# Optimization experiments

Hardware: AMD Instinct MI355X
Metric: run time of the kernel (lower is better)

Reference implementation:

```python
import jax, jax.numpy as jnp
import numpy as np

N, E, DIN, H, M, O = 100000, 3200000, 128, 256, 500, 100


def setup_inputs() -> dict:
    key = jax.random.key(0)
    ks = jax.random.split(key, 8)
    x = jax.random.normal(ks[0], (N, DIN), dtype=jnp.float32)
    edge_index = jax.random.randint(ks[1], (2, E), 0, N, dtype=jnp.int64)
    # GCNConv weights (glorot-ish scale) and biases
    W1 = jax.random.normal(ks[2], (DIN, H), dtype=jnp.float32) / np.sqrt(DIN)
    b1 = jnp.zeros((H,), dtype=jnp.float32)
    W2 = jax.random.normal(ks[3], (H, M), dtype=jnp.float32) / np.sqrt(H)
    b2 = jnp.zeros((M,), dtype=jnp.float32)
    # output head ('GO'): Linear(M -> O)
    Wout = jax.random.normal(ks[4], (M, O), dtype=jnp.float32) / np.sqrt(M)
    bout = jnp.zeros((O,), dtype=jnp.float32)
    # threshold param stored as inv_softplus(1.0) so softplus(threshold)=1.0
    threshold = jnp.float32(np.log(np.expm1(1.0)))
    return {"x": x, "edge_index": edge_index, "W1": W1, "b1": b1,
            "W2": W2, "b2": b2, "Wout": Wout, "bout": bout,
            "threshold": threshold}


def reference(x, edge_index, W1, b1, W2, b2, Wout, bout, threshold):
    src, dst = edge_index[0], edge_index[1]
    n = x.shape[0]
    # GCN sym-normalization with improved=True (self-loop weight 2):
    # deg[i] = 2 + #incoming edges; norm(e) = deg^-1/2[src] * deg^-1/2[dst]
    deg = jax.ops.segment_sum(jnp.ones(src.shape[0], x.dtype), dst,
                              num_segments=n) + jnp.asarray(2.0, x.dtype)
    dinv = jax.lax.rsqrt(deg)
    coef = dinv[src] * dinv[dst]              # [E]
    self_coef = (2.0 * dinv * dinv)[:, None]  # [N,1] self-loop term

    def gcn_conv(h, W, b):
        h = h @ W                              # [N,C]
        agg = jax.ops.segment_sum(h[src] * coef[:, None], dst, num_segments=n)
        return agg + self_coef * h + b

    h = jax.nn.relu(gcn_conv(x, W1, b1))       # conv + ReLU (no bn, no dropout)
    module_representation = jax.nn.softplus(gcn_conv(h, W2, b2))  # [N,M]
    # tanh probability transform: tanh(softplus(threshold) * x)
    p = jnp.tanh(jax.nn.softplus(threshold) * module_representation)
    y_go = p @ Wout + bout                     # output head 'GO'
    return (module_representation, y_go)
```

## Files before the change

kernel.cpp:

```cpp
#include <hip/hip_runtime.h>
#include <cstdint>
#include <cstddef>

#define DIN 128
#define HID 256
#define MODD 500
#define OUTD 100

typedef unsigned int uint;
typedef unsigned short ushort;
typedef __attribute__((ext_vector_type(8))) __bf16 bf16x8;
typedef __attribute__((ext_vector_type(4))) float f32x4;

__device__ __forceinline__ float bf2f(ushort u) {
    return __uint_as_float(((uint)u) << 16);
}
__device__ __forceinline__ ushort f2bf(float f) {
    uint u = __float_as_uint(f);
    return (ushort)((u + 0x7FFF + ((u >> 16) & 1)) >> 16);
}
__device__ __forceinline__ void async_copy16(const void* g, void* l) {
    __builtin_amdgcn_global_load_lds((const __attribute__((address_space(1))) void*)g,
                                     (__attribute__((address_space(3))) void*)l, 16, 0, 0);
}
__device__ __forceinline__ float tanh_fast(float x) {
    return 1.0f - 2.0f / (__expf(2.0f * x) + 1.0f);
}
__device__ __forceinline__ float softplus_fast(float v) {
    return fmaxf(v, 0.0f) + __logf(1.0f + __expf(-fabsf(v)));
}


__global__ void count_deg(const int* __restrict__ dst, int* __restrict__ deg, int E) {
    int e = blockIdx.x * blockDim.x + threadIdx.x;
    if (e < E) atomicAdd(&deg[dst[e]], 1);
}

__global__ void compute_dinv(const int* __restrict__ deg, float* __restrict__ dinv, int N) {
    int i = blockIdx.x * blockDim.x + threadIdx.x;
    if (i < N) dinv[i] = rsqrtf((float)deg[i] + 2.0f);
}

__global__ void scan_block(const int* __restrict__ deg, int* __restrict__ rp,
                           int* __restrict__ bsum, int n) {
    __shared__ int wsum[16];
    int tid = threadIdx.x;
    int lane = tid & 63;
    int w = tid >> 6;
    int i = blockIdx.x * 1024 + tid;
    int v = (i < n) ? deg[i] : 0;
    int x = v;
    #pragma unroll
    for (int off = 1; off < 64; off <<= 1) {
        int t = __shfl_up(x, off);
        if (lane >= off) x += t;
    }
    if (lane == 63) wsum[w] = x;
    __syncthreads();
    if (tid == 0) {
        int s = 0;
        #pragma unroll
        for (int k = 0; k < 16; ++k) { int t = wsum[k]; wsum[k] = s; s += t; }
        bsum[blockIdx.x] = s;
    }
    __syncthreads();
    if (i < n) rp[i] = wsum[w] + (x - v);
}

__global__ void scan_bsums(int* __restrict__ bsum, int nb) {
    if (threadIdx.x == 0 && blockIdx.x == 0) {
        int s = 0;
        for (int k = 0; k < nb; ++k) { int t = bsum[k]; bsum[k] = s; s += t; }
        bsum[nb] = s;
    }
}

__global__ void scan_add(int* __restrict__ rp, const int* __restrict__ bsum, int n, int nb) {
    int i = blockIdx.x * blockDim.x + threadIdx.x;
    if (i < n) rp[i] += bsum[i >> 10];
    else if (i == n) rp[n] = bsum[nb];
}


#define BSH 9
#define MAXB 256
#define PCH 8192

__global__ void init_bucket_cursor(const int* __restrict__ rp, int* __restrict__ bcur,
                                   int NB) {
    int b = blockIdx.x * blockDim.x + threadIdx.x;
    if (b < NB) bcur[b] = rp[b << BSH];
}

__global__ __launch_bounds__(256)
void partition_edges(const int* __restrict__ src, const int* __restrict__ dst,
                     int* __restrict__ bcur, uint* __restrict__ pairBuf,
                     int E, int NB) {
    __shared__ int hist[MAXB];
    __shared__ int gbase[MAXB];
    int tid = threadIdx.x;
    int e0 = blockIdx.x * PCH;
    int e1 = min(e0 + PCH, E);
    for (int b = tid; b < NB; b += 256) hist[b] = 0;
    __syncthreads();
    for (int e = e0 + tid; e < e1; e += 256) {
        int d = dst[e];
        atomicAdd(&hist[d >> BSH], 1);
    }
    __syncthreads();
    for (int b = tid; b < NB; b += 256) {
        int h = hist[b];
        gbase[b] = h ? atomicAdd(&bcur[b], h) : 0;
        hist[b] = 0;
    }
    __syncthreads();
    for (int e = e0 + tid; e < e1; e += 256) {
        int d = dst[e];
        int s = src[e];
        int b = d >> BSH;
        int idx = gbase[b] + atomicAdd(&hist[b], 1);
        pairBuf[idx] = (uint)s | ((uint)(d & ((1 << BSH) - 1)) << 20);
    }
}

__global__ __launch_bounds__(512)
void bucket_scatter(const uint* __restrict__ pairBuf, const int* __restrict__ rp,
                    int* __restrict__ col, int N) {
    __shared__ int lcur[1 << BSH];
    int b = blockIdx.x;
    int n0 = b << BSH;
    int nn = min(1 << BSH, N - n0);
    int tid = threadIdx.x;
    for (int i = tid; i < nn; i += 512) lcur[i] = rp[n0 + i];
    __syncthreads();
    int start = rp[n0];
    int end = rp[min(n0 + (1 << BSH), N)];
    for (int e = start + tid; e < end; e += 512) {
        uint v = pairBuf[e];
        int doff = v >> 20;
        int s = v & 0xFFFFF;
        int pos = atomicAdd(&lcur[doff], 1);
        col[pos] = s;
    }
}


__global__ void cast_f32_bf16(const float* __restrict__ src, ushort* __restrict__ dst, int n4) {
    int i = blockIdx.x * blockDim.x + threadIdx.x;
    if (i < n4) {
        float4 v = ((const float4*)src)[i];
        ushort4 o;
        o.x = f2bf(v.x); o.y = f2bf(v.y); o.z = f2bf(v.z); o.w = f2bf(v.w);
        ((ushort4*)dst)[i] = o;
    }
}

__global__ void transpose_cast(const float* __restrict__ src, ushort* __restrict__ dst,
                               int K, int N, int Kpad, int Npad) {
    int idx = blockIdx.x * blockDim.x + threadIdx.x;
    if (idx >= Npad * Kpad) return;
    int n = idx / Kpad, k = idx - n * Kpad;
    float v = (n < N && k < K) ? src[(size_t)k * N + n] : 0.0f;
    dst[idx] = f2bf(v);
}


__global__ void aggregate128(const ushort* __restrict__ X, ushort* __restrict__ Y,
                             const int* __restrict__ rp, const int* __restrict__ col,
                             const float* __restrict__ dinv, int N) {
    int gw = blockIdx.x * (blockDim.x >> 6) + (threadIdx.x >> 6);
    int lane = threadIdx.x & 63;
    if (gw >= N) return;
    float di = dinv[gw];
    float sc = 2.0f * di * di;
    const uint* Xr = (const uint*)X;
    uint s = Xr[(size_t)gw * 64 + lane];
    float ax = sc * bf2f((ushort)(s & 0xFFFF));
    float ay = sc * bf2f((ushort)(s >> 16));
    int e = rp[gw], end = rp[gw + 1];
    for (; e + 2 <= end; e += 2) {
        int c0 = col[e], c1 = col[e + 1];
        float w0 = dinv[c0] * di, w1 = dinv[c1] * di;
        uint v0 = Xr[(size_t)c0 * 64 + lane];
        uint v1 = Xr[(size_t)c1 * 64 + lane];
        ax += w0 * bf2f((ushort)(v0 & 0xFFFF));
        ay += w0 * bf2f((ushort)(v0 >> 16));
        ax += w1 * bf2f((ushort)(v1 & 0xFFFF));
        ay += w1 * bf2f((ushort)(v1 >> 16));
    }
    if (e < end) {
        int c0 = col[e];
        float w0 = dinv[c0] * di;
        uint v0 = Xr[(size_t)c0 * 64 + lane];
        ax += w0 * bf2f((ushort)(v0 & 0xFFFF));
        ay += w0 * bf2f((ushort)(v0 >> 16));
    }
    uint out = (uint)f2bf(ax) | ((uint)f2bf(ay) << 16);
    ((uint*)Y)[(size_t)gw * 64 + lane] = out;
}

__global__ void aggregate256(const ushort* __restrict__ X, ushort* __restrict__ Y,
                             const int* __restrict__ rp, const int* __restrict__ col,
                             const float* __restrict__ dinv, int N) {
    int gw = blockIdx.x * (blockDim.x >> 6) + (threadIdx.x >> 6);
    int lane = threadIdx.x & 63;
    if (gw >= N) return;
    float di = dinv[gw];
    float sc = 2.0f * di * di;
    const uint2* Xr = (const uint2*)X;
    uint2 s = Xr[(size_t)gw * 64 + lane];
    float a0 = sc * bf2f((ushort)(s.x & 0xFFFF));
    float a1 = sc * bf2f((ushort)(s.x >> 16));
    float a2 = sc * bf2f((ushort)(s.y & 0xFFFF));
    float a3 = sc * bf2f((ushort)(s.y >> 16));
    int e = rp[gw], end = rp[gw + 1];
    for (; e + 2 <= end; e += 2) {
        int c0 = col[e], c1 = col[e + 1];
        float w0 = dinv[c0] * di, w1 = dinv[c1] * di;
        uint2 v0 = Xr[(size_t)c0 * 64 + lane];
        uint2 v1 = Xr[(size_t)c1 * 64 + lane];
        a0 += w0 * bf2f((ushort)(v0.x & 0xFFFF));
        a1 += w0 * bf2f((ushort)(v0.x >> 16));
        a2 += w0 * bf2f((ushort)(v0.y & 0xFFFF));
        a3 += w0 * bf2f((ushort)(v0.y >> 16));
        a0 += w1 * bf2f((ushort)(v1.x & 0xFFFF));
        a1 += w1 * bf2f((ushort)(v1.x >> 16));
        a2 += w1 * bf2f((ushort)(v1.y & 0xFFFF));
        a3 += w1 * bf2f((ushort)(v1.y >> 16));
    }
    if (e < end) {
        int c0 = col[e];
        float w0 = dinv[c0] * di;
        uint2 v0 = Xr[(size_t)c0 * 64 + lane];
        a0 += w0 * bf2f((ushort)(v0.x & 0xFFFF));
        a1 += w0 * bf2f((ushort)(v0.x >> 16));
        a2 += w0 * bf2f((ushort)(v0.y & 0xFFFF));
        a3 += w0 * bf2f((ushort)(v0.y >> 16));
    }
    uint2 out;
    out.x = (uint)f2bf(a0) | ((uint)f2bf(a1) << 16);
    out.y = (uint)f2bf(a2) | ((uint)f2bf(a3) << 16);
    ((uint2*)Y)[(size_t)gw * 64 + lane] = out;
}


template<int K, int MODE>
__global__ __launch_bounds__(256)
void gemm_bt(const ushort* __restrict__ A, const ushort* __restrict__ BT,
             const float* __restrict__ bias, void* __restrict__ Cout,
             int M, int Nact, int ldc) {
    __shared__ ushort sA[128 * 32];
    __shared__ ushort sB[128 * 32];
    int tid = threadIdx.x;
    int lane = tid & 63;
    int w = tid >> 6;
    int wr = w >> 1, wc = w & 1;
    int row0 = blockIdx.y * 128;
    int col0 = blockIdx.x * 128;
    f32x4 acc[4][4] = {};

    for (int kt = 0; kt < K; kt += 32) {
        if (kt) __syncthreads();
        #pragma unroll
        for (int L = 0; L < 2; ++L) {
            int cb = L * 256 + w * 64;
            int c = cb + lane;
            int r = c >> 2;
            int ko = (c & 3) * 8;
            int rr = min(row0 + r, M - 1);
            async_copy16(A + (size_t)rr * K + kt + ko, sA + (size_t)cb * 8);
        }
        #pragma unroll
        for (int L = 0; L < 2; ++L) {
            int cb = L * 256 + w * 64;
            int c = cb + lane;
            int nr = c >> 2;
            int ko = (c & 3) * 8;
            async_copy16(BT + (size_t)(col0 + nr) * K + kt + ko, sB + (size_t)cb * 8);
        }
        __syncthreads();
        bf16x8 af[4], bfr[4];
        #pragma unroll
        for (int i = 0; i < 4; ++i) {
            int row = wr * 64 + i * 16 + (lane & 15);
            af[i] = *(const bf16x8*)(sA + row * 32 + (lane >> 4) * 8);
        }
        #pragma unroll
        for (int j = 0; j < 4; ++j) {
            int n = wc * 64 + j * 16 + (lane & 15);
            bfr[j] = *(const bf16x8*)(sB + n * 32 + (lane >> 4) * 8);
        }
        #pragma unroll
        for (int i = 0; i < 4; ++i)
            #pragma unroll
            for (int j = 0; j < 4; ++j)
                acc[i][j] = __builtin_amdgcn_mfma_f32_16x16x32_bf16(af[i], bfr[j], acc[i][j], 0, 0, 0);
    }

    #pragma unroll
    for (int i = 0; i < 4; ++i) {
        #pragma unroll
        for (int j = 0; j < 4; ++j) {
            int col = col0 + wc * 64 + j * 16 + (lane & 15);
            if (col >= Nact) continue;
            float bv = bias[col];
            #pragma unroll
            for (int r = 0; r < 4; ++r) {
                int row = row0 + wr * 64 + i * 16 + (lane >> 4) * 4 + r;
                if (row >= M) continue;
                float v = acc[i][j][r] + bv;
                if (MODE == 0) {
                    v = fmaxf(v, 0.0f);
                    ((ushort*)Cout)[(size_t)row * ldc + col] = f2bf(v);
                } else if (MODE == 1) {
                    v = softplus_fast(v);
                    ((float*)Cout)[(size_t)row * ldc + col] = v;
                } else {
                    ((float*)Cout)[(size_t)row * ldc + col] = v;
                }
            }
        }
    }
}

__global__ __launch_bounds__(256)
void gemm_tanh(const float* __restrict__ Ain, const ushort* __restrict__ BT,
               const float* __restrict__ bias, float* __restrict__ Cout,
               int M, int Nact, int ldc, const float* __restrict__ thr) {
    const int K = 512, KA = 500;
    __shared__ ushort sA[128 * 32];
    __shared__ ushort sB[128 * 32];
    int tid = threadIdx.x;
    int lane = tid & 63;
    int w = tid >> 6;
    int wr = w >> 1, wc = w & 1;
    int row0 = blockIdx.y * 128;
    int col0 = blockIdx.x * 128;
    float t = *thr;
    float sp = softplus_fast(t);
    f32x4 acc[4][4] = {};

    int r = tid >> 1;
    int kh = (tid & 1) * 16;
    int rr_a = min(row0 + r, M - 1);
    const float* arow = Ain + (size_t)rr_a * KA;

    for (int kt = 0; kt < K; kt += 32) {
        if (kt) __syncthreads();
        float vals[16];
        int kb = kt + kh;
        if (kb + 16 <= KA) {
            #pragma unroll
            for (int q = 0; q < 4; ++q) {
                float4 f = *(const float4*)(arow + kb + q * 4);
                vals[q * 4 + 0] = f.x; vals[q * 4 + 1] = f.y;
                vals[q * 4 + 2] = f.z; vals[q * 4 + 3] = f.w;
            }
        } else {
            #pragma unroll
            for (int q = 0; q < 16; ++q) {
                int k = kb + q;
                vals[q] = (k < KA) ? arow[k] : 0.0f;
            }
        }
        ushort us[16];
        #pragma unroll
        for (int q = 0; q < 16; ++q) us[q] = f2bf(tanh_fast(sp * vals[q]));
        *(uint4*)(sA + r * 32 + kh) = *(const uint4*)(us);
        *(uint4*)(sA + r * 32 + kh + 8) = *(const uint4*)(us + 8);
        #pragma unroll
        for (int L = 0; L < 2; ++L) {
            int cb = L * 256 + w * 64;
            int c = cb + lane;
            int nr = c >> 2;
            int ko = (c & 3) * 8;
            async_copy16(BT + (size_t)(col0 + nr) * K + kt + ko, sB + (size_t)cb * 8);
        }
        __syncthreads();
        bf16x8 af[4], bfr[4];
        #pragma unroll
        for (int i = 0; i < 4; ++i) {
            int row = wr * 64 + i * 16 + (lane & 15);
            af[i] = *(const bf16x8*)(sA + row * 32 + (lane >> 4) * 8);
        }
        #pragma unroll
        for (int j = 0; j < 4; ++j) {
            int n = wc * 64 + j * 16 + (lane & 15);
            bfr[j] = *(const bf16x8*)(sB + n * 32 + (lane >> 4) * 8);
        }
        #pragma unroll
        for (int i = 0; i < 4; ++i)
            #pragma unroll
            for (int j = 0; j < 4; ++j)
                acc[i][j] = __builtin_amdgcn_mfma_f32_16x16x32_bf16(af[i], bfr[j], acc[i][j], 0, 0, 0);
    }

    #pragma unroll
    for (int i = 0; i < 4; ++i) {
        #pragma unroll
        for (int j = 0; j < 4; ++j) {
            int col = col0 + wc * 64 + j * 16 + (lane & 15);
            if (col >= Nact) continue;
            float bv = bias[col];
            #pragma unroll
            for (int rix = 0; rix < 4; ++rix) {
                int row = row0 + wr * 64 + i * 16 + (lane >> 4) * 4 + rix;
                if (row >= M) continue;
                Cout[(size_t)row * ldc + col] = acc[i][j][rix] + bv;
            }
        }
    }
}


extern "C" void kernel_launch(void* const* d_in, const int* in_sizes, int n_in,
                              void* d_out, int out_size, void* d_ws, size_t ws_size,
                              hipStream_t stream) {
    const float* x    = (const float*)d_in[0];
    const int*   ei   = (const int*)d_in[1];
    const float* W1   = (const float*)d_in[2];
    const float* b1   = (const float*)d_in[3];
    const float* W2   = (const float*)d_in[4];
    const float* b2   = (const float*)d_in[5];
    const float* Wout = (const float*)d_in[6];
    const float* bout = (const float*)d_in[7];
    const float* thr  = (const float*)d_in[8];

    int N = in_sizes[0] / DIN;
    int E = in_sizes[1] / 2;
    const int* srcI = ei;
    const int* dstI = ei + E;

    char* wsp = (char*)d_ws;
    size_t o = 0;
    auto alloc = [&](size_t bytes) -> void* {
        void* p = wsp + o;
        o = (o + bytes + 255) & ~(size_t)255;
        return p;
    };
    int*    deg   = (int*)alloc((size_t)N * 4);
    float*  dinv  = (float*)alloc((size_t)N * 4);
    int*    rp    = (int*)alloc((size_t)(N + 1) * 4);
    int*    bsum  = (int*)alloc(1024);
    int*    bcur  = (int*)alloc(MAXB * 4);
    int*    col   = (int*)alloc((size_t)E * 4);
    ushort* W1T   = (ushort*)alloc((size_t)256 * 128 * 2);
    ushort* W2T   = (ushort*)alloc((size_t)512 * 256 * 2);
    ushort* WoutT = (ushort*)alloc((size_t)128 * 512 * 2);
    ushort* bufA  = (ushort*)alloc((size_t)N * 256 * 2);
    ushort* hbuf  = (ushort*)alloc((size_t)N * 256 * 2);

    ushort* xbf = bufA;
    ushort* xa  = bufA + (size_t)N * 128;
    ushort* ha  = bufA;
    uint* pairBuf = (uint*)hbuf;

    float* mr   = (float*)d_out;
    float* yout = (float*)d_out + (size_t)N * MODD;

    int mtiles = (N + 127) / 128;
    int NB = (N + (1 << BSH) - 1) >> BSH;

    hipMemsetAsync(deg, 0, (size_t)N * 4, stream);
    count_deg<<<(E + 255) / 256, 256, 0, stream>>>(dstI, deg, E);
    compute_dinv<<<(N + 255) / 256, 256, 0, stream>>>(deg, dinv, N);
    int nb = (N + 1023) / 1024;
    scan_block<<<nb, 1024, 0, stream>>>(deg, rp, bsum, N);
    scan_bsums<<<1, 64, 0, stream>>>(bsum, nb);
    scan_add<<<(N + 256) / 256, 256, 0, stream>>>(rp, bsum, N, nb);
    init_bucket_cursor<<<1, 256, 0, stream>>>(rp, bcur, NB);
    partition_edges<<<(E + PCH - 1) / PCH, 256, 0, stream>>>(srcI, dstI, bcur, pairBuf, E, NB);
    bucket_scatter<<<NB, 512, 0, stream>>>(pairBuf, rp, col, N);

    cast_f32_bf16<<<((N * DIN / 4) + 255) / 256, 256, 0, stream>>>(x, xbf, N * DIN / 4);
    transpose_cast<<<(256 * 128 + 255) / 256, 256, 0, stream>>>(W1, W1T, 128, 256, 128, 256);
    transpose_cast<<<(512 * 256 + 255) / 256, 256, 0, stream>>>(W2, W2T, 256, 500, 256, 512);
    transpose_cast<<<(128 * 512 + 255) / 256, 256, 0, stream>>>(Wout, WoutT, 500, 100, 512, 128);

    aggregate128<<<(N + 3) / 4, 256, 0, stream>>>(xbf, xa, rp, col, dinv, N);
    gemm_bt<128, 0><<<dim3(2, mtiles), 256, 0, stream>>>(xa, W1T, b1, hbuf, N, HID, HID);

    aggregate256<<<(N + 3) / 4, 256, 0, stream>>>(hbuf, ha, rp, col, dinv, N);
    gemm_bt<256, 1><<<dim3(4, mtiles), 256, 0, stream>>>(ha, W2T, b2, mr, N, MODD, MODD);

    gemm_tanh<<<dim3(1, mtiles), 256, 0, stream>>>(mr, WoutT, bout, yout, N, OUTD, OUTD, thr);
}
```

Measured before the change: 1.140 ms.

## Vectorize aggregation with edge-parallel lane groups and fuse tanh into layer-2 GEMM epilogue

The two aggregation kernels now load 16-byte rows, with subgroups of lanes processing different neighbor edges in parallel and combining partial sums by cross-lane shuffles. This gives wider memory transactions and more outstanding gathers per wavefront. The layer-2 GEMM epilogue also writes tanh(softplus(thr)*v) as a padded bf16 buffer, so the output head becomes a plain async-copy GEMM instead of re-reading the fp32 representation and applying tanh in its load path. The cost is an extra N×512 bf16 write and read through a buffer that aliases the col/hbuf workspace, plus some idle lanes in the aggregation tail handling.

```diff
diff --git a/kernel.cpp b/kernel.cpp
--- a/kernel.cpp
+++ b/kernel.cpp
@@ -19,6 +19,9 @@
     uint u = __float_as_uint(f);
     return (ushort)((u + 0x7FFF + ((u >> 16) & 1)) >> 16);
 }
+__device__ __forceinline__ uint packbf2(float lo, float hi) {
+    return (uint)f2bf(lo) | ((uint)f2bf(hi) << 16);
+}
 __device__ __forceinline__ void async_copy16(const void* g, void* l) {
     __builtin_amdgcn_global_load_lds((const __attribute__((address_space(1))) void*)g,
                                      (__attribute__((address_space(3))) void*)l, 16, 0, 0);
@@ -28,6 +31,16 @@
 }
 __device__ __forceinline__ float softplus_fast(float v) {
     return fmaxf(v, 0.0f) + __logf(1.0f + __expf(-fabsf(v)));
+}
+__device__ __forceinline__ void acc8(float* a, uint4 v, float w) {
+    a[0] += w * bf2f((ushort)(v.x & 0xFFFF));
+    a[1] += w * bf2f((ushort)(v.x >> 16));
+    a[2] += w * bf2f((ushort)(v.y & 0xFFFF));
+    a[3] += w * bf2f((ushort)(v.y >> 16));
+    a[4] += w * bf2f((ushort)(v.z & 0xFFFF));
+    a[5] += w * bf2f((ushort)(v.z >> 16));
+    a[6] += w * bf2f((ushort)(v.w & 0xFFFF));
+    a[7] += w * bf2f((ushort)(v.w >> 16));
 }
 
 
@@ -171,32 +184,49 @@
     int gw = blockIdx.x * (blockDim.x >> 6) + (threadIdx.x >> 6);
     int lane = threadIdx.x & 63;
     if (gw >= N) return;
+    int g = lane >> 4;
+    int sub = lane & 15;
     float di = dinv[gw];
     float sc = 2.0f * di * di;
-    const uint* Xr = (const uint*)X;
-    uint s = Xr[(size_t)gw * 64 + lane];
-    float ax = sc * bf2f((ushort)(s & 0xFFFF));
-    float ay = sc * bf2f((ushort)(s >> 16));
+    const uint4* Xr = (const uint4*)X;
+    float a[8] = {};
+    if (g == 0) acc8(a, Xr[(size_t)gw * 16 + sub], sc);
     int e = rp[gw], end = rp[gw + 1];
-    for (; e + 2 <= end; e += 2) {
-        int c0 = col[e], c1 = col[e + 1];
+    int base = e;
+    for (; base + 8 <= end; base += 8) {
+        int c0 = col[base + g];
+        int c1 = col[base + 4 + g];
         float w0 = dinv[c0] * di, w1 = dinv[c1] * di;
-        uint v0 = Xr[(size_t)c0 * 64 + lane];
-        uint v1 = Xr[(size_t)c1 * 64 + lane];
-        ax += w0 * bf2f((ushort)(v0 & 0xFFFF));
-        ay += w0 * bf2f((ushort)(v0 >> 16));
-        ax += w1 * bf2f((ushort)(v1 & 0xFFFF));
-        ay += w1 * bf2f((ushort)(v1 >> 16));
-    }
-    if (e < end) {
-        int c0 = col[e];
+        uint4 v0 = Xr[(size_t)c0 * 16 + sub];
+        uint4 v1 = Xr[(size_t)c1 * 16 + sub];
+        acc8(a, v0, w0);
+        acc8(a, v1, w1);
+    }
+    if (base + 4 <= end) {
+        int c0 = col[base + g];
         float w0 = dinv[c0] * di;
-        uint v0 = Xr[(size_t)c0 * 64 + lane];
-        ax += w0 * bf2f((ushort)(v0 & 0xFFFF));
-        ay += w0 * bf2f((ushort)(v0 >> 16));
-    }
-    uint out = (uint)f2bf(ax) | ((uint)f2bf(ay) << 16);
-    ((uint*)Y)[(size_t)gw * 64 + lane] = out;
+        acc8(a, Xr[(size_t)c0 * 16 + sub], w0);
+        base += 4;
+    }
+    int rem = end - base;
+    if (g < rem) {
+        int c0 = col[base + g];
+        float w0 = dinv[c0] * di;
+        acc8(a, Xr[(size_t)c0 * 16 + sub], w0);
+    }
+    #pragma unroll
+    for (int q = 0; q < 8; ++q) {
+        a[q] += __shfl_xor(a[q], 16);
+        a[q] += __shfl_xor(a[q], 32);
+    }
+    if (g == 0) {
+        uint4 o;
+        o.x = packbf2(a[0], a[1]);
+        o.y = packbf2(a[2], a[3]);
+        o.z = packbf2(a[4], a[5]);
+        o.w = packbf2(a[6], a[7]);
+        ((uint4*)Y)[(size_t)gw * 16 + sub] = o;
+    }
 }
 
 __global__ void aggregate256(const ushort* __restrict__ X, ushort* __restrict__ Y,
@@ -205,42 +235,45 @@
     int gw = blockIdx.x * (blockDim.x >> 6) + (threadIdx.x >> 6);
     int lane = threadIdx.x & 63;
     if (gw >= N) return;
+    int g = lane >> 5;
+    int sub = lane & 31;
     float di = dinv[gw];
     float sc = 2.0f * di * di;
-    const uint2* Xr = (const uint2*)X;
-    uint2 s = Xr[(size_t)gw * 64 + lane];
-    float a0 = sc * bf2f((ushort)(s.x & 0xFFFF));
-    float a1 = sc * bf2f((ushort)(s.x >> 16));
-    float a2 = sc * bf2f((ushort)(s.y & 0xFFFF));
-    float a3 = sc * bf2f((ushort)(s.y >> 16));
+    const uint4* Xr = (const uint4*)X;
+    float a[8] = {};
+    if (g == 0) acc8(a, Xr[(size_t)gw * 32 + sub], sc);
     int e = rp[gw], end = rp[gw + 1];
-    for (; e + 2 <= end; e += 2) {
-        int c0 = col[e], c1 = col[e + 1];
+    int base = e;
+    for (; base + 4 <= end; base += 4) {
+        int c0 = col[base + g];
+        int c1 = col[base + 2 + g];
         float w0 = dinv[c0] * di, w1 = dinv[c1] * di;
-        uint2 v0 = Xr[(size_t)c0 * 64 + lane];
-        uint2 v1 = Xr[(size_t)c1 * 64 + lane];
-        a0 += w0 * bf2f((ushort)(v0.x & 0xFFFF));
-        a1 += w0 * bf2f((ushort)(v0.x >> 16));
-        a2 += w0 * bf2f((ushort)(v0.y & 0xFFFF));
-        a3 += w0 * bf2f((ushort)(v0.y >> 16));
-        a0 += w1 * bf2f((ushort)(v1.x & 0xFFFF));
-        a1 += w1 * bf2f((ushort)(v1.x >> 16));
-        a2 += w1 * bf2f((ushort)(v1.y & 0xFFFF));
-        a3 += w1 * bf2f((ushort)(v1.y >> 16));
-    }
-    if (e < end) {
-        int c0 = col[e];
+        uint4 v0 = Xr[(size_t)c0 * 32 + sub];
+        uint4 v1 = Xr[(size_t)c1 * 32 + sub];
+        acc8(a, v0, w0);
+        acc8(a, v1, w1);
+    }
+    if (base + 2 <= end) {
+        int c0 = col[base + g];
         float w0 = dinv[c0] * di;
-        uint2 v0 = Xr[(size_t)c0 * 64 + lane];
-        a0 += w0 * bf2f((ushort)(v0.x & 0xFFFF));
-        a1 += w0 * bf2f((ushort)(v0.x >> 16));
-        a2 += w0 * bf2f((ushort)(v0.y & 0xFFFF));
-        a3 += w0 * bf2f((ushort)(v0.y >> 16));
-    }
-    uint2 out;
-    out.x = (uint)f2bf(a0) | ((uint)f2bf(a1) << 16);
-    out.y = (uint)f2bf(a2) | ((uint)f2bf(a3) << 16);
-    ((uint2*)Y)[(size_t)gw * 64 + lane] = out;
+        acc8(a, Xr[(size_t)c0 * 32 + sub], w0);
+        base += 2;
+    }
+    if (base < end && g == 0) {
+        int c0 = col[base];
+        float w0 = dinv[c0] * di;
+        acc8(a, Xr[(size_t)c0 * 32 + sub], w0);
+    }
+    #pragma unroll
+    for (int q = 0; q < 8; ++q) a[q] += __shfl_xor(a[q], 32);
+    if (g == 0) {
+        uint4 o;
+        o.x = packbf2(a[0], a[1]);
+        o.y = packbf2(a[2], a[3]);
+        o.z = packbf2(a[4], a[5]);
+        o.w = packbf2(a[6], a[7]);
+        ((uint4*)Y)[(size_t)gw * 32 + sub] = o;
+    }
 }
 
 
@@ -248,7 +281,8 @@
 __global__ __launch_bounds__(256)
 void gemm_bt(const ushort* __restrict__ A, const ushort* __restrict__ BT,
              const float* __restrict__ bias, void* __restrict__ Cout,
-             int M, int Nact, int ldc) {
+             int M, int Nact, int ldc, ushort* __restrict__ C2,
+             const float* __restrict__ thr) {
     __shared__ ushort sA[128 * 32];
     __shared__ ushort sB[128 * 32];
     int tid = threadIdx.x;
@@ -257,6 +291,8 @@
     int wr = w >> 1, wc = w & 1;
     int row0 = blockIdx.y * 128;
     int col0 = blockIdx.x * 128;
+    float sp = 0.0f;
+    if (MODE == 3) sp = softplus_fast(*thr);
     f32x4 acc[4][4] = {};
 
     for (int kt = 0; kt < K; kt += 32) {
@@ -302,111 +338,36 @@
         #pragma unroll
         for (int j = 0; j < 4; ++j) {
             int col = col0 + wc * 64 + j * 16 + (lane & 15);
-            if (col >= Nact) continue;
-            float bv = bias[col];
-            #pragma unroll
-            for (int r = 0; r < 4; ++r) {
-                int row = row0 + wr * 64 + i * 16 + (lane >> 4) * 4 + r;
-                if (row >= M) continue;
-                float v = acc[i][j][r] + bv;
-                if (MODE == 0) {
-                    v = fmaxf(v, 0.0f);
-                    ((ushort*)Cout)[(size_t)row * ldc + col] = f2bf(v);
-                } else if (MODE == 1) {
-                    v = softplus_fast(v);
-                    ((float*)Cout)[(size_t)row * ldc + col] = v;
-                } else {
-                    ((float*)Cout)[(size_t)row * ldc + col] = v;
+            if (MODE == 3) {
+                bool act = (col < Nact);
+                float bv = act ? bias[col] : 0.0f;
+                #pragma unroll
+                for (int r = 0; r < 4; ++r) {
+                    int row = row0 + wr * 64 + i * 16 + (lane >> 4) * 4 + r;
+                    if (row >= M) continue;
+                    if (act) {
+                        float v = softplus_fast(acc[i][j][r] + bv);
+                        ((float*)Cout)[(size_t)row * ldc + col] = v;
+                        C2[(size_t)row * 512 + col] = f2bf(tanh_fast(sp * v));
+                    } else {
+                        C2[(size_t)row * 512 + col] = 0;
+                    }
                 }
-            }
-        }
-    }
-}
-
-__global__ __launch_bounds__(256)
-void gemm_tanh(const float* __restrict__ Ain, const ushort* __restrict__ BT,
-               const float* __restrict__ bias, float* __restrict__ Cout,
-               int M, int Nact, int ldc, const float* __restrict__ thr) {
-    const int K = 512, KA = 500;
-    __shared__ ushort sA[128 * 32];
-    __shared__ ushort sB[128 * 32];
-    int tid = threadIdx.x;
-    int lane = tid & 63;
-    int w = tid >> 6;
-    int wr = w >> 1, wc = w & 1;
-    int row0 = blockIdx.y * 128;
-    int col0 = blockIdx.x * 128;
-    float t = *thr;
-    float sp = softplus_fast(t);
-    f32x4 acc[4][4] = {};
-
-    int r = tid >> 1;
-    int kh = (tid & 1) * 16;
-    int rr_a = min(row0 + r, M - 1);
-    const float* arow = Ain + (size_t)rr_a * KA;
-
-    for (int kt = 0; kt < K; kt += 32) {
-        if (kt) __syncthreads();
-        float vals[16];
-        int kb = kt + kh;
-        if (kb + 16 <= KA) {
-            #pragma unroll
-            for (int q = 0; q < 4; ++q) {
-                float4 f = *(const float4*)(arow + kb + q * 4);
-                vals[q * 4 + 0] = f.x; vals[q * 4 + 1] = f.y;
-                vals[q * 4 + 2] = f.z; vals[q * 4 + 3] = f.w;
-            }
-        } else {
-            #pragma unroll
-            for (int q = 0; q < 16; ++q) {
-                int k = kb + q;
-                vals[q] = (k < KA) ? arow[k] : 0.0f;
-            }
-        }
-        ushort us[16];
-        #pragma unroll
-        for (int q = 0; q < 16; ++q) us[q] = f2bf(tanh_fast(sp * vals[q]));
-        *(uint4*)(sA + r * 32 + kh) = *(const uint4*)(us);
-        *(uint4*)(sA + r * 32 + kh + 8) = *(const uint4*)(us + 8);
-        #pragma unroll
-        for (int L = 0; L < 2; ++L) {
-            int cb = L * 256 + w * 64;
-            int c = cb + lane;
-            int nr = c >> 2;
-            int ko = (c & 3) * 8;
-            async_copy16(BT + (size_t)(col0 + nr) * K + kt + ko, sB + (size_t)cb * 8);
-        }
-        __syncthreads();
-        bf16x8 af[4], bfr[4];
-        #pragma unroll
-        for (int i = 0; i < 4; ++i) {
-            int row = wr * 64 + i * 16 + (lane & 15);
-            af[i] = *(const bf16x8*)(sA + row * 32 + (lane >> 4) * 8);
-        }
-        #pragma unroll
-        for (int j = 0; j < 4; ++j) {
-            int n = wc * 64 + j * 16 + (lane & 15);
-            bfr[j] = *(const bf16x8*)(sB + n * 32 + (lane >> 4) * 8);
-        }
-        #pragma unroll
-        for (int i = 0; i < 4; ++i)
-            #pragma unroll
-            for (int j = 0; j < 4; ++j)
-                acc[i][j] = __builtin_amdgcn_mfma_f32_16x16x32_bf16(af[i], bfr[j], acc[i][j], 0, 0, 0);
-    }
-
-    #pragma unroll
-    for (int i = 0; i < 4; ++i) {
-        #pragma unroll
-        for (int j = 0; j < 4; ++j) {
-            int col = col0 + wc * 64 + j * 16 + (lane & 15);
-            if (col >= Nact) continue;
-            float bv = bias[col];
-            #pragma unroll
-            for (int rix = 0; rix < 4; ++rix) {
-                int row = row0 + wr * 64 + i * 16 + (lane >> 4) * 4 + rix;
-                if (row >= M) continue;
-                Cout[(size_t)row * ldc + col] = acc[i][j][rix] + bv;
+            } else {
+                if (col >= Nact) continue;
+                float bv = bias[col];
+                #pragma unroll
+                for (int r = 0; r < 4; ++r) {
+                    int row = row0 + wr * 64 + i * 16 + (lane >> 4) * 4 + r;
+                    if (row >= M) continue;
+                    float v = acc[i][j][r] + bv;
+                    if (MODE == 0) {
+                        v = fmaxf(v, 0.0f);
+                        ((ushort*)Cout)[(size_t)row * ldc + col] = f2bf(v);
+                    } else {
+                        ((float*)Cout)[(size_t)row * ldc + col] = v;
+                    }
+                }
             }
         }
     }
@@ -443,12 +404,16 @@
     int*    rp    = (int*)alloc((size_t)(N + 1) * 4);
     int*    bsum  = (int*)alloc(1024);
     int*    bcur  = (int*)alloc(MAXB * 4);
-    int*    col   = (int*)alloc((size_t)E * 4);
     ushort* W1T   = (ushort*)alloc((size_t)256 * 128 * 2);
     ushort* W2T   = (ushort*)alloc((size_t)512 * 256 * 2);
     ushort* WoutT = (ushort*)alloc((size_t)128 * 512 * 2);
     ushort* bufA  = (ushort*)alloc((size_t)N * 256 * 2);
+    size_t  col_off = o;
+    int*    col   = (int*)alloc((size_t)E * 4);
     ushort* hbuf  = (ushort*)alloc((size_t)N * 256 * 2);
+    size_t  pbf_need = col_off + (size_t)N * 512 * 2;
+    if (o < pbf_need) o = (pbf_need + 255) & ~(size_t)255;
+    ushort* pbf = (ushort*)(wsp + col_off);
 
     ushort* xbf = bufA;
     ushort* xa  = bufA + (size_t)N * 128;
@@ -478,10 +443,13 @@
     transpose_cast<<<(128 * 512 + 255) / 256, 256, 0, stream>>>(Wout, WoutT, 500, 100, 512, 128);
 
     aggregate128<<<(N + 3) / 4, 256, 0, stream>>>(xbf, xa, rp, col, dinv, N);
-    gemm_bt<128, 0><<<dim3(2, mtiles), 256, 0, stream>>>(xa, W1T, b1, hbuf, N, HID, HID);
+    gemm_bt<128, 0><<<dim3(2, mtiles), 256, 0, stream>>>(xa, W1T, b1, hbuf, N, HID, HID,
+                                                         nullptr, nullptr);
 
     aggregate256<<<(N + 3) / 4, 256, 0, stream>>>(hbuf, ha, rp, col, dinv, N);
-    gemm_bt<256, 1><<<dim3(4, mtiles), 256, 0, stream>>>(ha, W2T, b2, mr, N, MODD, MODD);
-
-    gemm_tanh<<<dim3(1, mtiles), 256, 0, stream>>>(mr, WoutT, bout, yout, N, OUTD, OUTD, thr);
-}
+    gemm_bt<256, 3><<<dim3(4, mtiles), 256, 0, stream>>>(ha, W2T, b2, mr, N, MODD, MODD,
+                                                         pbf, thr);
+
+    gemm_bt<512, 2><<<dim3(1, mtiles), 256, 0, stream>>>(pbf, WoutT, bout, yout, N, OUTD, OUTD,
+                                                         nullptr, nullptr);
+}
```

After: 1.072 ms. -5.9%, faster.
